# Performance work log

Measured on AMD Instinct MI355X. Metric: run time of the kernel, lower is better.

## Reference

```python
import jax, jax.numpy as jnp
import numpy as np

TEMPERATURE = 0.5
MAX_PAIRS = 50
EPS = 1e-12


def _build_pair_indices(sids, max_pairs=MAX_PAIRS):
    """Replicates the original nested-Python-loop pair enumeration order,
    with early exit (valid because the original truncates to the FIRST
    max_pairs pairs in the same enumeration order)."""
    uniq = np.unique(sids)  # torch.unique returns sorted uniques
    idx_by = {s: np.nonzero(sids == s)[0] for s in uniq}
    pos_i, pos_j, neg_i, neg_j = [], [], [], []
    for s in uniq:
        ti = idx_by[s]
        if len(ti) >= 2 and len(pos_i) < max_pairs:
            for a in range(len(ti)):
                for b in range(a + 1, len(ti)):
                    if len(pos_i) < max_pairs:
                        pos_i.append(ti[a]); pos_j.append(ti[b])
        for o in uniq:
            if o == s:
                continue
            if len(neg_i) >= max_pairs:
                break
            tj = idx_by[o]
            for a in ti:
                for b in tj:
                    if len(neg_i) < max_pairs:
                        neg_i.append(a); neg_j.append(b)
        if len(pos_i) >= max_pairs and len(neg_i) >= max_pairs:
            break
    return (np.asarray(pos_i, dtype=np.int32), np.asarray(pos_j, dtype=np.int32),
            np.asarray(neg_i, dtype=np.int32), np.asarray(neg_j, dtype=np.int32))


def _l2_normalize(x, axis=1):
    # matches F.normalize: x / max(||x||, eps)
    n = jnp.sqrt(jnp.sum(x * x, axis=axis, keepdims=True))
    return x / jnp.maximum(n, EPS)


def setup_inputs() -> dict:
    key = jax.random.key(0)
    k1, k2 = jax.random.split(key)
    B, D = 65536, 384
    identity_tokens = jax.random.normal(k1, (B, D), dtype=jnp.float32)
    subject_ids = jax.random.randint(k2, (B,), 0, 1024, dtype=jnp.int64)
    return {"identity_tokens": identity_tokens, "subject_ids": subject_ids}


def reference(identity_tokens, subject_ids):
    # pair indices are a pure function of the (constant) integer subject ids;
    # computed host-side in numpy, exactly mirroring the torch loop order
    pi, pj, ni, nj = _build_pair_indices(np.asarray(subject_ids))
    n_pos, n_neg = len(pi), len(ni)
    ii = jnp.asarray(np.concatenate([pi, ni]))
    jj = jnp.asarray(np.concatenate([pj, nj]))

    # full-batch normalize (as in forward), then gather selected rows
    z = _l2_normalize(identity_tokens, axis=1)  # [B, 384]
    zi = _l2_normalize(z[ii], axis=1)           # second normalize: matches
    zj = _l2_normalize(z[jj], axis=1)           # contrastive_loss_with_pairs

    sims = jnp.sum(zi * zj, axis=1) / TEMPERATURE  # [n_pos + n_neg]
    labels = jnp.concatenate([jnp.ones((n_pos,), jnp.float32),
                              jnp.zeros((n_neg,), jnp.float32)])
    # binary_cross_entropy_with_logits, mean reduction (numerically stable)
    loss = -jnp.mean(labels * jax.nn.log_sigmoid(sims)
                     + (1.0 - labels) * jax.nn.log_sigmoid(-sims))
    return loss
```

## Files before the change

### kernel.cpp

```cpp
#include <hip/hip_runtime.h>
#include <math.h>

#define NSUB 1024
#define CAP 128
#define MAXP 50
#define TEMP_INV 2.0f
#define EPSN 1e-12f


__global__ void k_hist(const int* __restrict__ sid32, int B,
                       int* __restrict__ cnt, int* __restrict__ idxbuf,
                       float* __restrict__ out) {
    int tid = threadIdx.x;
    if (blockIdx.x == 0 && tid == 0) out[0] = 0.0f;
    int i = blockIdx.x * blockDim.x + tid;
    int w = (i < B) ? sid32[i] : 0;
    int odd_nz = ((tid & 1) && (i < B) && (w != 0)) ? 1 : 0;
    int is32 = __syncthreads_or(odd_nz);
    if (i >= B) return;
    int s = is32 ? w : sid32[2 * i];
    if ((unsigned)s < (unsigned)NSUB) {
        int slot = atomicAdd(&cnt[s], 1);
        if (slot < CAP) idxbuf[s * CAP + slot] = i;
    }
}

__global__ __launch_bounds__(128)
void k_pair(const float* __restrict__ X, int D,
            const int* __restrict__ cnt, const int* __restrict__ idxbuf,
            float* __restrict__ out) {
    __shared__ int ls[NSUB];
    __shared__ short ps_s[MAXP], ps_a[MAXP], ps_b[MAXP];
    __shared__ short ng_s[MAXP], ng_a[MAXP], ng_o[MAXP], ng_b[MAXP];
    __shared__ int sh_npos, sh_ntot;
    __shared__ int Li[CAP], Lj[CAP];
    __shared__ int sh_rowi, sh_rowj;
    __shared__ float r0[2], r1[2], r2[2];

    int t = threadIdx.x;
    for (int k = t; k < NSUB; k += 128) ls[k] = cnt[k];
    __syncthreads();

    if (t == 0) {
        int n_pos = 0, n_neg = 0;
        for (int s = 0; s < NSUB; ++s) {
            int m = ls[s];
            if (m == 0) continue;
            if (m >= 2 && n_pos < MAXP) {
                for (int a = 0; a < m && n_pos < MAXP; ++a)
                    for (int b = a + 1; b < m && n_pos < MAXP; ++b) {
                        ps_s[n_pos] = (short)s; ps_a[n_pos] = (short)a;
                        ps_b[n_pos] = (short)b; ++n_pos;
                    }
            }
            for (int o = 0; o < NSUB; ++o) {
                if (o == s) continue;
                int n = ls[o];
                if (n == 0) continue;
                if (n_neg >= MAXP) break;
                for (int a = 0; a < m && n_neg < MAXP; ++a)
                    for (int b = 0; b < n && n_neg < MAXP; ++b) {
                        ng_s[n_neg] = (short)s; ng_a[n_neg] = (short)a;
                        ng_o[n_neg] = (short)o; ng_b[n_neg] = (short)b;
                        ++n_neg;
                    }
            }
            if (n_pos >= MAXP && n_neg >= MAXP) break;
        }
        sh_npos = n_pos; sh_ntot = n_pos + n_neg;
    }
    __syncthreads();

    int p = blockIdx.x;
    int n_pos = sh_npos, n_tot = sh_ntot;
    if (p >= n_tot) return;

    int si, ri, sj, rj;
    if (p < n_pos) { si = ps_s[p]; ri = ps_a[p]; sj = ps_s[p]; rj = ps_b[p]; }
    else {
        int q = p - n_pos;
        si = ng_s[q]; ri = ng_a[q]; sj = ng_o[q]; rj = ng_b[q];
    }

    int ni = min(ls[si], CAP);
    int nj = min(ls[sj], CAP);
    if (t < ni) Li[t] = idxbuf[si * CAP + t];
    if (t < nj) Lj[t] = idxbuf[sj * CAP + t];
    __syncthreads();
    if (t < ni) {
        int v = Li[t], r = 0;
        for (int k = 0; k < ni; ++k) r += (Li[k] < v) ? 1 : 0;
        if (r == ri) sh_rowi = v;
    }
    if (t < nj) {
        int v = Lj[t], r = 0;
        for (int k = 0; k < nj; ++k) r += (Lj[k] < v) ? 1 : 0;
        if (r == rj) sh_rowj = v;
    }
    __syncthreads();

    const float* xi = X + (size_t)sh_rowi * (size_t)D;
    const float* xj = X + (size_t)sh_rowj * (size_t)D;
    float dij = 0.f, dii = 0.f, djj = 0.f;
    #pragma unroll 3
    for (int k = t; k < D; k += 128) {
        float a = xi[k], b = xj[k];
        dij += a * b; dii += a * a; djj += b * b;
    }
    #pragma unroll
    for (int off = 32; off >= 1; off >>= 1) {
        dij += __shfl_xor(dij, off, 64);
        dii += __shfl_xor(dii, off, 64);
        djj += __shfl_xor(djj, off, 64);
    }
    int w = t >> 6, lane = t & 63;
    if (lane == 0) { r0[w] = dij; r1[w] = dii; r2[w] = djj; }
    __syncthreads();
    if (t == 0) {
        dij = r0[0] + r0[1]; dii = r1[0] + r1[1]; djj = r2[0] + r2[1];
        float nrmi = sqrtf(dii), nrmj = sqrtf(djj);
        float d1i = fmaxf(nrmi, EPSN), d1j = fmaxf(nrmj, EPSN);
        float d2i = fmaxf(nrmi / d1i, EPSN), d2j = fmaxf(nrmj / d1j, EPSN);
        float sim = dij / (d1i * d2i * d1j * d2j) * TEMP_INV;
        float x = (p < n_pos) ? -sim : sim;
        float term = fmaxf(x, 0.f) + log1pf(expf(-fabsf(x)));
        atomicAdd(out, term / (float)n_tot);
    }
}

extern "C" void kernel_launch(void* const* d_in, const int* in_sizes, int n_in,
                              void* d_out, int out_size, void* d_ws, size_t ws_size,
                              hipStream_t stream) {
    const float* X = (const float*)d_in[0];
    const int* sid32 = (const int*)d_in[1];
    float* out = (float*)d_out;

    int B = in_sizes[1];
    int D = in_sizes[0] / B;

    int* cnt = (int*)d_ws;
    int* idxbuf = (int*)((char*)d_ws + 8192);

    hipMemsetAsync(cnt, 0, 4096, stream);
    k_hist<<<(B + 255) / 256, 256, 0, stream>>>(sid32, B, cnt, idxbuf, out);
    k_pair<<<2 * MAXP, 128, 0, stream>>>(X, D, cnt, idxbuf, out);
}
```

Measured before the change: 144.6 us.

## Fuse memset, histogram and pair kernels into one cooperative launch

Replaces the memset plus two kernel launches with a single cooperative kernel that uses grid-wide syncs between zeroing, histogram building, and pair evaluation. Counters are padded to a 16-int stride so the histogram atomics on different subjects do not share cache lines. The pair stage now runs with 256 threads per block. The aim is to cut launch overhead and atomic contention. In exchange it adds the cost of grid.sync across 256 blocks, and cooperative launch needs every block to be resident at once.

```diff
diff --git a/kernel.cpp b/kernel.cpp
--- a/kernel.cpp
+++ b/kernel.cpp
@@ -1,44 +1,56 @@
 #include <hip/hip_runtime.h>
+#include <hip/hip_cooperative_groups.h>
 #include <math.h>
+
+namespace cg = cooperative_groups;
 
 #define NSUB 1024
 #define CAP 128
 #define MAXP 50
 #define TEMP_INV 2.0f
 #define EPSN 1e-12f
+#define CSTRIDE 16
 
 
-__global__ void k_hist(const int* __restrict__ sid32, int B,
-                       int* __restrict__ cnt, int* __restrict__ idxbuf,
-                       float* __restrict__ out) {
-    int tid = threadIdx.x;
-    if (blockIdx.x == 0 && tid == 0) out[0] = 0.0f;
-    int i = blockIdx.x * blockDim.x + tid;
-    int w = (i < B) ? sid32[i] : 0;
-    int odd_nz = ((tid & 1) && (i < B) && (w != 0)) ? 1 : 0;
-    int is32 = __syncthreads_or(odd_nz);
-    if (i >= B) return;
-    int s = is32 ? w : sid32[2 * i];
-    if ((unsigned)s < (unsigned)NSUB) {
-        int slot = atomicAdd(&cnt[s], 1);
-        if (slot < CAP) idxbuf[s * CAP + slot] = i;
+__global__ __launch_bounds__(256)
+void k_fused(const float* __restrict__ X, int D,
+             const int* __restrict__ sid32, int B,
+             int* __restrict__ cntP, int* __restrict__ idxbuf,
+             float* __restrict__ out) {
+    cg::grid_group grid = cg::this_grid();
+    int t = threadIdx.x;
+    int gid = blockIdx.x * blockDim.x + t;
+
+    if (gid < NSUB) cntP[gid * CSTRIDE] = 0;
+    if (gid == 0) out[0] = 0.0f;
+    grid.sync();
+
+    {
+        int i = gid;
+        int w = (i < B) ? sid32[i] : 0;
+        int odd_nz = ((t & 1) && (i < B) && (w != 0)) ? 1 : 0;
+        int is32 = __syncthreads_or(odd_nz);
+        if (i < B) {
+            int s = is32 ? w : sid32[2 * i];
+            if ((unsigned)s < (unsigned)NSUB) {
+                int slot = atomicAdd(&cntP[s * CSTRIDE], 1);
+                if (slot < CAP) idxbuf[s * CAP + slot] = i;
+            }
+        }
     }
-}
+    grid.sync();
 
-__global__ __launch_bounds__(128)
-void k_pair(const float* __restrict__ X, int D,
-            const int* __restrict__ cnt, const int* __restrict__ idxbuf,
-            float* __restrict__ out) {
     __shared__ int ls[NSUB];
     __shared__ short ps_s[MAXP], ps_a[MAXP], ps_b[MAXP];
     __shared__ short ng_s[MAXP], ng_a[MAXP], ng_o[MAXP], ng_b[MAXP];
     __shared__ int sh_npos, sh_ntot;
     __shared__ int Li[CAP], Lj[CAP];
     __shared__ int sh_rowi, sh_rowj;
-    __shared__ float r0[2], r1[2], r2[2];
+    __shared__ float r0[4], r1[4], r2[4];
 
-    int t = threadIdx.x;
-    for (int k = t; k < NSUB; k += 128) ls[k] = cnt[k];
+    if (blockIdx.x >= 2 * MAXP) return;
+
+    for (int k = t; k < NSUB; k += 256) ls[k] = cntP[k * CSTRIDE];
     __syncthreads();
 
     if (t == 0) {
@@ -102,8 +114,8 @@
     const float* xi = X + (size_t)sh_rowi * (size_t)D;
     const float* xj = X + (size_t)sh_rowj * (size_t)D;
     float dij = 0.f, dii = 0.f, djj = 0.f;
-    #pragma unroll 3
-    for (int k = t; k < D; k += 128) {
+    #pragma unroll 2
+    for (int k = t; k < D; k += 256) {
         float a = xi[k], b = xj[k];
         dij += a * b; dii += a * a; djj += b * b;
     }
@@ -113,11 +125,13 @@
         dii += __shfl_xor(dii, off, 64);
         djj += __shfl_xor(djj, off, 64);
     }
-    int w = t >> 6, lane = t & 63;
-    if (lane == 0) { r0[w] = dij; r1[w] = dii; r2[w] = djj; }
+    int wv = t >> 6, lane = t & 63;
+    if (lane == 0) { r0[wv] = dij; r1[wv] = dii; r2[wv] = djj; }
     __syncthreads();
     if (t == 0) {
-        dij = r0[0] + r0[1]; dii = r1[0] + r1[1]; djj = r2[0] + r2[1];
+        dij = r0[0] + r0[1] + r0[2] + r0[3];
+        dii = r1[0] + r1[1] + r1[2] + r1[3];
+        djj = r2[0] + r2[1] + r2[2] + r2[3];
         float nrmi = sqrtf(dii), nrmj = sqrtf(djj);
         float d1i = fmaxf(nrmi, EPSN), d1j = fmaxf(nrmj, EPSN);
         float d2i = fmaxf(nrmi / d1i, EPSN), d2j = fmaxf(nrmj / d1j, EPSN);
@@ -138,10 +152,14 @@
     int B = in_sizes[1];
     int D = in_sizes[0] / B;
 
-    int* cnt = (int*)d_ws;
-    int* idxbuf = (int*)((char*)d_ws + 8192);
+    int* cntP = (int*)d_ws;
+    int* idxbuf = (int*)((char*)d_ws + 65536);
 
-    hipMemsetAsync(cnt, 0, 4096, stream);
-    k_hist<<<(B + 255) / 256, 256, 0, stream>>>(sid32, B, cnt, idxbuf, out);
-    k_pair<<<2 * MAXP, 128, 0, stream>>>(X, D, cnt, idxbuf, out);
+    int nblk = (B + 255) / 256;
+    if (nblk < 2 * MAXP) nblk = 2 * MAXP;
+
+    void* args[] = {(void*)&X, (void*)&D, (void*)&sid32, (void*)&B,
+                    (void*)&cntP, (void*)&idxbuf, (void*)&out};
+    hipLaunchCooperativeKernel((const void*)k_fused, dim3(nblk), dim3(256),
+                               args, 0, stream);
 }
```

After: 191.4 us. +32.3%, slower.
